# Performance work log

Hardware: AMD Instinct MI355X
Metric: run time of the kernel (lower is better)

Reference implementation:

```python
import jax, jax.numpy as jnp
import numpy as np

DIM = 256
NUM_HEADS = 4
HEAD_DIM = DIM // NUM_HEADS
EPS = 1e-5


def setup_inputs() -> dict:
    key = jax.random.key(0)
    ks = jax.random.split(key, 8)
    B, N, C = 8, 2048, DIM
    s = 0.02
    return {
        "x": jax.random.normal(ks[0], (B, N, C), jnp.float32),
        "qkv_w": jax.random.normal(ks[1], (C, 3 * C), jnp.float32) * s,
        "qkv_b": jnp.zeros((3 * C,), jnp.float32),
        "proj_w": jax.random.normal(ks[2], (C, C), jnp.float32) * s,
        "proj_b": jnp.zeros((C,), jnp.float32),
        "ln1_g": jnp.ones((C,), jnp.float32),
        "ln1_b": jnp.zeros((C,), jnp.float32),
        "ln2_g": jnp.ones((C,), jnp.float32),
        "ln2_b": jnp.zeros((C,), jnp.float32),
        "mlp_w1": jax.random.normal(ks[3], (C, 2 * C), jnp.float32) * s,
        "mlp_b1": jnp.zeros((2 * C,), jnp.float32),
        "mlp_w2": jax.random.normal(ks[4], (2 * C, C), jnp.float32) * s,
        "mlp_b2": jnp.zeros((C,), jnp.float32),
    }


def _layernorm(x, g, b):
    mu = jnp.mean(x, axis=-1, keepdims=True)
    var = jnp.mean(jnp.square(x - mu), axis=-1, keepdims=True)
    return (x - mu) * jax.lax.rsqrt(var + EPS) * g + b


def reference(x, qkv_w, qkv_b, proj_w, proj_b, ln1_g, ln1_b, ln2_g, ln2_b,
              mlp_w1, mlp_b1, mlp_w2, mlp_b2):
    B, N, C = x.shape
    H, D = NUM_HEADS, HEAD_DIM
    shortcut = x
    h = _layernorm(x, ln1_g, ln1_b)
    qkv = (h @ qkv_w + qkv_b).reshape(B, N, 3, H, D)
    q = qkv[:, :, 0].transpose(0, 2, 1, 3)  # [B,H,N,D]
    k = qkv[:, :, 1].transpose(0, 2, 1, 3)
    v = qkv[:, :, 2].transpose(0, 2, 1, 3)
    attn = jnp.einsum('bhnd,bhmd->bhnm', q, k) * (D ** -0.5)
    attn = jax.nn.softmax(attn, axis=-1)  # dropout = identity (eval mode)
    o = jnp.einsum('bhnm,bhmd->bhnd', attn, v)
    o = o.transpose(0, 2, 1, 3).reshape(B, N, C)
    x = o @ proj_w + proj_b + shortcut
    h2 = _layernorm(x, ln2_g, ln2_b)
    mlp = jax.nn.gelu(h2 @ mlp_w1 + mlp_b1, approximate=False) @ mlp_w2 + mlp_b2
    return x + mlp
```

## Files before the change

kernel.cpp:

```cpp
#include <hip/hip_runtime.h>

typedef __bf16 bf16;
typedef __bf16 bf16x8 __attribute__((ext_vector_type(8)));
typedef __bf16 bf16x4 __attribute__((ext_vector_type(4)));
typedef float  f32x4  __attribute__((ext_vector_type(4)));

typedef __attribute__((address_space(1))) const void GASV;
typedef __attribute__((address_space(3))) void LASV;

__device__ __forceinline__ void gload16(const void* g, void* l) {
  __builtin_amdgcn_global_load_lds((GASV*)g, (LASV*)l, 16, 0, 0);
}

__global__ __launch_bounds__(256) void wconv_t(const float* __restrict__ in,
                                               bf16* __restrict__ out,
                                               int lgK, int Cin, int total) {
  int idx = blockIdx.x * 256 + threadIdx.x;
  if (idx >= total) return;
  int K = 1 << lgK;
  int k = idx & (K - 1);
  int n = idx >> lgK;
  out[idx] = (bf16)in[(size_t)k * Cin + n];
}

__global__ __launch_bounds__(256) void ln_fwd(const float* __restrict__ x,
                                              const float* __restrict__ gam,
                                              const float* __restrict__ bet,
                                              bf16* __restrict__ out) {
  const int lane = threadIdx.x & 63;
  const int w = threadIdx.x >> 6;
  const size_t row = (size_t)blockIdx.x * 4 + w;
  const float4 v = *(const float4*)(x + row * 256 + lane * 4);
  float s1 = v.x + v.y + v.z + v.w;
  float s2 = v.x * v.x + v.y * v.y + v.z * v.z + v.w * v.w;
#pragma unroll
  for (int m = 1; m < 64; m <<= 1) {
    s1 += __shfl_xor(s1, m);
    s2 += __shfl_xor(s2, m);
  }
  const float mu = s1 * (1.0f / 256.0f);
  const float var = s2 * (1.0f / 256.0f) - mu * mu;
  const float rs = rsqrtf(var + 1e-5f);
  const float4 g4 = *(const float4*)(gam + lane * 4);
  const float4 b4 = *(const float4*)(bet + lane * 4);
  bf16x4 o;
  o[0] = (bf16)((v.x - mu) * rs * g4.x + b4.x);
  o[1] = (bf16)((v.y - mu) * rs * g4.y + b4.y);
  o[2] = (bf16)((v.z - mu) * rs * g4.z + b4.z);
  o[3] = (bf16)((v.w - mu) * rs * g4.w + b4.w);
  *(bf16x4*)(out + row * 256 + lane * 4) = o;
}

template <int EPI>
__global__ __launch_bounds__(256) void gemm_bt(const bf16* __restrict__ A,
                                               const bf16* __restrict__ Bt,
                                               const float* __restrict__ bias,
                                               const float* __restrict__ res,
                                               void* __restrict__ outp,
                                               int M, int N, int K) {
  __shared__ bf16 Al[2][8192];
  __shared__ bf16 Bl[2][8192];
  const int tid = threadIdx.x;
  const int lane = tid & 63;
  const int wid = tid >> 6;
  const int wm = wid >> 1, wn = wid & 1;
  const int nbm = M >> 7;
  const int bm = (int)blockIdx.x % nbm;
  const int bn = (int)blockIdx.x / nbm;
  const int m0 = bm << 7, n0 = bn << 7;
  const int nk = K >> 6;

  f32x4 acc[4][4];
#pragma unroll
  for (int i = 0; i < 4; ++i)
#pragma unroll
    for (int j = 0; j < 4; ++j) acc[i][j] = (f32x4){0.f, 0.f, 0.f, 0.f};

  auto stage = [&](int t, int s) {
    const int k0 = t << 6;
#pragma unroll
    for (int p = 0; p < 4; ++p) {
      const int idx = p * 4096 + tid * 16;
      const int row = idx >> 7;
      const int colb = idx & 127;
      gload16((const char*)(A + ((size_t)(m0 + row) * K + k0)) + colb,
              (char*)&Al[s][0] + p * 4096 + ((tid >> 6) << 10));
      gload16((const char*)(Bt + ((size_t)(n0 + row) * K + k0)) + colb,
              (char*)&Bl[s][0] + p * 4096 + ((tid >> 6) << 10));
    }
  };

  stage(0, 0);
  asm volatile("s_waitcnt vmcnt(0)" ::: "memory");
  __syncthreads();

  for (int t = 0; t < nk; ++t) {
    if (t + 1 < nk) stage(t + 1, (t + 1) & 1);
    const bf16* pa = &Al[t & 1][0] + (wm * 64 + (lane & 15)) * 64 + ((lane >> 4) << 3);
    const bf16* pb = &Bl[t & 1][0] + (wn * 64 + (lane & 15)) * 64 + ((lane >> 4) << 3);
    bf16x8 av[4][2], bv[4][2];
#pragma unroll
    for (int f = 0; f < 4; ++f)
#pragma unroll
      for (int ks = 0; ks < 2; ++ks) {
        av[f][ks] = *(const bf16x8*)(pa + f * 1024 + ks * 32);
        bv[f][ks] = *(const bf16x8*)(pb + f * 1024 + ks * 32);
      }
#pragma unroll
    for (int fm = 0; fm < 4; ++fm)
#pragma unroll
      for (int fn = 0; fn < 4; ++fn) {
        acc[fm][fn] = __builtin_amdgcn_mfma_f32_16x16x32_bf16(av[fm][0], bv[fn][0], acc[fm][fn], 0, 0, 0);
        acc[fm][fn] = __builtin_amdgcn_mfma_f32_16x16x32_bf16(av[fm][1], bv[fn][1], acc[fm][fn], 0, 0, 0);
      }
    asm volatile("s_waitcnt vmcnt(0)" ::: "memory");
    __syncthreads();
  }

#pragma unroll
  for (int fm = 0; fm < 4; ++fm)
#pragma unroll
    for (int fn = 0; fn < 4; ++fn) {
      const int r0 = m0 + wm * 64 + fm * 16 + ((lane >> 4) << 2);
      const int c = n0 + wn * 64 + fn * 16 + (lane & 15);
#pragma unroll
      for (int j = 0; j < 4; ++j) {
        const int r = r0 + j;
        const float v = acc[fm][fn][j];
        if constexpr (EPI == 0) {
          ((bf16*)outp)[(size_t)r * N + c] = (bf16)(v + bias[c]);
        } else if constexpr (EPI == 1) {
          ((bf16*)outp)[(size_t)r * 2048 + ((size_t)(c >> 11)) * 524288 + (c & 2047)] =
              (bf16)(v + bias[r]);
        } else if constexpr (EPI == 2) {
          ((float*)outp)[(size_t)r * N + c] = v + bias[c] + res[(size_t)r * N + c];
        } else {
          const float u = v + bias[c];
          ((bf16*)outp)[(size_t)r * N + c] = (bf16)(u * 0.5f * (1.0f + erff(u * 0.70710678118f)));
        }
      }
    }
}

__global__ __launch_bounds__(256) void attn_fwd(const bf16* __restrict__ qk,
                                                const bf16* __restrict__ vT,
                                                bf16* __restrict__ ob) {
  __shared__ bf16 Kl[2][4096];
  __shared__ bf16 Vl[2][4096];
  const int tid = threadIdx.x;
  const int lane = tid & 63;
  const int w = tid >> 6;
  const int g = lane >> 4;
  const int qi = lane & 15;
  const int bh = blockIdx.x & 31;
  const int qt = blockIdx.x >> 5;
  const int b = bh >> 2, h = bh & 3;

  const size_t qrow = (size_t)b * 2048 + qt * 64 + w * 16 + qi;
  const bf16* qp = qk + qrow * 512 + h * 64 + g * 8;
  const bf16x8 qf0 = *(const bf16x8*)qp;
  const bf16x8 qf1 = *(const bf16x8*)(qp + 32);

  float mrun = -1e30f, lsum = 0.0f;
  f32x4 o[4];
#pragma unroll
  for (int i = 0; i < 4; ++i) o[i] = (f32x4){0.f, 0.f, 0.f, 0.f};

  const char* kbase = (const char*)qk + ((size_t)b * 2048) * 1024 + 512 + h * 128;
  const char* vbase = (const char*)vT + (size_t)bh * 262144;
  constexpr float CEXP = 0.125f * 1.44269504088896340736f;

  auto stage = [&](int t, int s) {
#pragma unroll
    for (int p = 0; p < 4; ++p) {
      const int idx = (p & 1) * 4096 + tid * 16;
      const int row = idx >> 7;
      const int colb = (idx ^ ((row & 7) << 4)) & 127;
      if (p < 2) {
        gload16(kbase + (size_t)(t * 64 + row) * 1024 + colb,
                (char*)&Kl[s][0] + (p & 1) * 4096 + ((tid >> 6) << 10));
      } else {
        gload16(vbase + (size_t)row * 4096 + t * 128 + colb,
                (char*)&Vl[s][0] + (p & 1) * 4096 + ((tid >> 6) << 10));
      }
    }
  };

  stage(0, 0);
  asm volatile("s_waitcnt vmcnt(0)" ::: "memory");
  __syncthreads();

  for (int t = 0; t < 32; ++t) {
    if (t < 31) stage(t + 1, (t + 1) & 1);
    const int s = t & 1;
    f32x4 st[4];
#pragma unroll
    for (int fk = 0; fk < 4; ++fk) {
      const int kvr = fk * 16 + qi;
      const char* kb = (const char*)&Kl[s][0] + kvr * 128;
      const int sw = (kvr & 7) << 4;
      const bf16x8 k0 = *(const bf16x8*)(kb + ((g * 16) ^ sw));
      const bf16x8 k1 = *(const bf16x8*)(kb + ((64 + g * 16) ^ sw));
      f32x4 z = (f32x4){0.f, 0.f, 0.f, 0.f};
      st[fk] = __builtin_amdgcn_mfma_f32_16x16x32_bf16(k0, qf0, z, 0, 0, 0);
      st[fk] = __builtin_amdgcn_mfma_f32_16x16x32_bf16(k1, qf1, st[fk], 0, 0, 0);
    }
    float mt = st[0][0];
#pragma unroll
    for (int fk = 0; fk < 4; ++fk)
#pragma unroll
      for (int j = 0; j < 4; ++j) mt = fmaxf(mt, st[fk][j]);
    mt = fmaxf(mt, __shfl_xor(mt, 16));
    mt = fmaxf(mt, __shfl_xor(mt, 32));
    const float mnew = fmaxf(mrun, mt);
    const float alpha = exp2f(CEXP * (mrun - mnew));
    float p[16];
    float ts = 0.f;
#pragma unroll
    for (int fk = 0; fk < 4; ++fk)
#pragma unroll
      for (int j = 0; j < 4; ++j) {
        const float pv = exp2f(CEXP * (st[fk][j] - mnew));
        p[fk * 4 + j] = pv;
        ts += pv;
      }
    ts += __shfl_xor(ts, 16);
    ts += __shfl_xor(ts, 32);
    lsum = lsum * alpha + ts;
    mrun = mnew;
    float aj[4];
#pragma unroll
    for (int j = 0; j < 4; ++j) aj[j] = __shfl(alpha, g * 4 + j);
#pragma unroll
    for (int fd = 0; fd < 4; ++fd)
#pragma unroll
      for (int j = 0; j < 4; ++j) o[fd][j] *= aj[j];
    unsigned pk[8];
#pragma unroll
    for (int fk = 0; fk < 4; ++fk)
#pragma unroll
      for (int jp = 0; jp < 2; ++jp) {
        union { bf16 hh[2]; unsigned u; } cv;
        cv.hh[0] = (bf16)p[fk * 4 + 2 * jp];
        cv.hh[1] = (bf16)p[fk * 4 + 2 * jp + 1];
        pk[fk * 2 + jp] = cv.u;
      }
#pragma unroll
    for (int ksl = 0; ksl < 2; ++ksl) {
      union { bf16x8 v; unsigned u[4]; } pa;
#pragma unroll
      for (int pp = 0; pp < 4; ++pp) {
        const int src = ((2 * (g & 1) + (pp >> 1)) << 4) | qi;
        const unsigned r0 = (unsigned)__shfl((int)pk[(ksl * 2) * 2 + (pp & 1)], src);
        const unsigned r1 = (unsigned)__shfl((int)pk[(ksl * 2 + 1) * 2 + (pp & 1)], src);
        pa.u[pp] = (g >> 1) ? r1 : r0;
      }
#pragma unroll
      for (int fd = 0; fd < 4; ++fd) {
        const int dr = fd * 16 + qi;
        const char* vb = (const char*)&Vl[s][0] + dr * 128;
        const bf16x8 vv = *(const bf16x8*)(vb + ((ksl * 64 + g * 16) ^ ((dr & 7) << 4)));
        o[fd] = __builtin_amdgcn_mfma_f32_16x16x32_bf16(pa.v, vv, o[fd], 0, 0, 0);
      }
    }
    asm volatile("s_waitcnt vmcnt(0)" ::: "memory");
    __syncthreads();
  }

  const float inv = 1.0f / lsum;
  float ij[4];
#pragma unroll
  for (int j = 0; j < 4; ++j) ij[j] = __shfl(inv, g * 4 + j);
  const size_t orow0 = (size_t)b * 2048 + qt * 64 + w * 16 + g * 4;
#pragma unroll
  for (int fd = 0; fd < 4; ++fd)
#pragma unroll
    for (int j = 0; j < 4; ++j)
      ob[(orow0 + j) * 256 + h * 64 + fd * 16 + qi] = (bf16)(o[fd][j] * ij[j]);
}

extern "C" void kernel_launch(void* const* d_in, const int* in_sizes, int n_in,
                              void* d_out, int out_size, void* d_ws, size_t ws_size,
                              hipStream_t stream) {
  const float* x      = (const float*)d_in[0];
  const float* qkv_w  = (const float*)d_in[1];
  const float* qkv_b  = (const float*)d_in[2];
  const float* proj_w = (const float*)d_in[3];
  const float* proj_b = (const float*)d_in[4];
  const float* ln1_g  = (const float*)d_in[5];
  const float* ln1_b  = (const float*)d_in[6];
  const float* ln2_g  = (const float*)d_in[7];
  const float* ln2_b  = (const float*)d_in[8];
  const float* mlp_w1 = (const float*)d_in[9];
  const float* mlp_b1 = (const float*)d_in[10];
  const float* mlp_w2 = (const float*)d_in[11];
  const float* mlp_b2 = (const float*)d_in[12];
  float* out = (float*)d_out;

  char* ws = (char*)d_ws;
  bf16* Wtqkv = (bf16*)(ws);
  bf16* WtP   = (bf16*)(ws + 393216);
  bf16* Wt1   = (bf16*)(ws + 524288);
  bf16* Wt2   = (bf16*)(ws + 786432);
  bf16* h     = (bf16*)(ws + 1048576);
  bf16* qkb   = (bf16*)(ws + 9437184);
  bf16* vT    = (bf16*)(ws + 26214400);
  bf16* obuf  = (bf16*)(ws + 34603008);
  float* x2   = (float*)(ws + 42991616);
  bf16* a1 = qkb;
  bf16* h2 = h;

  wconv_t<<<768, 256, 0, stream>>>(qkv_w, Wtqkv, 8, 768, 196608);
  wconv_t<<<256, 256, 0, stream>>>(proj_w, WtP, 8, 256, 65536);
  wconv_t<<<512, 256, 0, stream>>>(mlp_w1, Wt1, 8, 512, 131072);
  wconv_t<<<512, 256, 0, stream>>>(mlp_w2, Wt2, 9, 256, 131072);

  ln_fwd<<<4096, 256, 0, stream>>>(x, ln1_g, ln1_b, h);
  gemm_bt<0><<<512, 256, 0, stream>>>(h, Wtqkv, qkv_b, nullptr, qkb, 16384, 512, 256);
  gemm_bt<1><<<256, 256, 0, stream>>>(Wtqkv + 512 * 256, h, qkv_b + 512, nullptr, vT, 256, 16384, 256);
  attn_fwd<<<1024, 256, 0, stream>>>(qkb, vT, obuf);
  gemm_bt<2><<<256, 256, 0, stream>>>(obuf, WtP, proj_b, x, x2, 16384, 256, 256);
  ln_fwd<<<4096, 256, 0, stream>>>(x2, ln2_g, ln2_b, h2);
  gemm_bt<3><<<512, 256, 0, stream>>>(h2, Wt1, mlp_b1, nullptr, a1, 16384, 512, 256);
  gemm_bt<2><<<256, 256, 0, stream>>>(a1, Wt2, mlp_b2, x2, out, 16384, 256, 512);
}
```

Before: 184.1 us.

## Restructure attention: transposed S layout, LDS P exchange, lazy rescale, MFMA priority

The attention kernel now computes S transposed so each lane owns one query column. That removes cross-lane shuffles for alpha and the final normalisation. P is passed through a per-wave LDS buffer instead of shuffle-based repacking, and K/V are staged into an MFMA-fragment-ordered LDS layout rather than an XOR-swizzled one. Online-softmax rescaling is skipped unless some row max grows past a threshold, and s_setprio is raised around MFMA blocks in both attention and GEMM. This adds LDS traffic and some numeric risk from deferred rescaling, which allows exponents up to 2^8 before bf16 conversion.

```diff
diff --git a/kernel.cpp b/kernel.cpp
--- a/kernel.cpp
+++ b/kernel.cpp
@@ -4,6 +4,7 @@
 typedef __bf16 bf16x8 __attribute__((ext_vector_type(8)));
 typedef __bf16 bf16x4 __attribute__((ext_vector_type(4)));
 typedef float  f32x4  __attribute__((ext_vector_type(4)));
+typedef unsigned u32x2 __attribute__((ext_vector_type(2)));
 
 typedef __attribute__((address_space(1))) const void GASV;
 typedef __attribute__((address_space(3))) void LASV;
@@ -106,6 +107,7 @@
         av[f][ks] = *(const bf16x8*)(pa + f * 1024 + ks * 32);
         bv[f][ks] = *(const bf16x8*)(pb + f * 1024 + ks * 32);
       }
+    __builtin_amdgcn_s_setprio(1);
 #pragma unroll
     for (int fm = 0; fm < 4; ++fm)
 #pragma unroll
@@ -113,6 +115,7 @@
         acc[fm][fn] = __builtin_amdgcn_mfma_f32_16x16x32_bf16(av[fm][0], bv[fn][0], acc[fm][fn], 0, 0, 0);
         acc[fm][fn] = __builtin_amdgcn_mfma_f32_16x16x32_bf16(av[fm][1], bv[fn][1], acc[fm][fn], 0, 0, 0);
       }
+    __builtin_amdgcn_s_setprio(0);
     asm volatile("s_waitcnt vmcnt(0)" ::: "memory");
     __syncthreads();
   }
@@ -147,6 +150,7 @@
                                                 bf16* __restrict__ ob) {
   __shared__ bf16 Kl[2][4096];
   __shared__ bf16 Vl[2][4096];
+  __shared__ bf16 Pl[4][1024];
   const int tid = threadIdx.x;
   const int lane = tid & 63;
   const int w = tid >> 6;
@@ -161,7 +165,7 @@
   const bf16x8 qf0 = *(const bf16x8*)qp;
   const bf16x8 qf1 = *(const bf16x8*)(qp + 32);
 
-  float mrun = -1e30f, lsum = 0.0f;
+  float mrun = 0.0f, lsum = 0.0f;
   f32x4 o[4];
 #pragma unroll
   for (int i = 0; i < 4; ++i) o[i] = (f32x4){0.f, 0.f, 0.f, 0.f};
@@ -169,20 +173,30 @@
   const char* kbase = (const char*)qk + ((size_t)b * 2048) * 1024 + 512 + h * 128;
   const char* vbase = (const char*)vT + (size_t)bh * 262144;
   constexpr float CEXP = 0.125f * 1.44269504088896340736f;
+  constexpr float THR = 8.0f / CEXP;
+
+  int koff[2], voff[2];
+#pragma unroll
+  for (int i = 0; i < 2; ++i) {
+    const int fk = i * 2 + (w >> 1);
+    const int half = w & 1;
+    koff[i] = (fk * 16 + qi) * 1024 + half * 64 + g * 16;
+    voff[i] = (fk * 16 + qi) * 4096 + half * 64 + g * 16;
+  }
+  char* const pw = (char*)&Pl[w][0];
+  int paddr[4];
+#pragma unroll
+  for (int fk = 0; fk < 4; ++fk)
+    paddr[fk] = (fk >> 1) * 1024 + ((fk & 1) * 2 + (g >> 1)) * 256 + qi * 16 + ((g & 1) * 2) * 4;
+  const char* const pr = (const char*)&Pl[w][0] + lane * 16;
 
   auto stage = [&](int t, int s) {
-#pragma unroll
-    for (int p = 0; p < 4; ++p) {
-      const int idx = (p & 1) * 4096 + tid * 16;
-      const int row = idx >> 7;
-      const int colb = (idx ^ ((row & 7) << 4)) & 127;
-      if (p < 2) {
-        gload16(kbase + (size_t)(t * 64 + row) * 1024 + colb,
-                (char*)&Kl[s][0] + (p & 1) * 4096 + ((tid >> 6) << 10));
-      } else {
-        gload16(vbase + (size_t)row * 4096 + t * 128 + colb,
-                (char*)&Vl[s][0] + (p & 1) * 4096 + ((tid >> 6) << 10));
-      }
+    const size_t kt = (size_t)t * 65536;
+    const size_t vt = (size_t)t * 128;
+#pragma unroll
+    for (int i = 0; i < 2; ++i) {
+      gload16(kbase + kt + koff[i], (char*)&Kl[s][0] + i * 4096 + w * 1024);
+      gload16(vbase + vt + voff[i], (char*)&Vl[s][0] + i * 4096 + w * 1024);
     }
   };
 
@@ -193,90 +207,85 @@
   for (int t = 0; t < 32; ++t) {
     if (t < 31) stage(t + 1, (t + 1) & 1);
     const int s = t & 1;
+    const char* kb = (const char*)&Kl[s][0] + lane * 16;
     f32x4 st[4];
+    __builtin_amdgcn_s_setprio(1);
 #pragma unroll
     for (int fk = 0; fk < 4; ++fk) {
-      const int kvr = fk * 16 + qi;
-      const char* kb = (const char*)&Kl[s][0] + kvr * 128;
-      const int sw = (kvr & 7) << 4;
-      const bf16x8 k0 = *(const bf16x8*)(kb + ((g * 16) ^ sw));
-      const bf16x8 k1 = *(const bf16x8*)(kb + ((64 + g * 16) ^ sw));
+      const bf16x8 k0 = *(const bf16x8*)(kb + fk * 2048);
+      const bf16x8 k1 = *(const bf16x8*)(kb + fk * 2048 + 1024);
       f32x4 z = (f32x4){0.f, 0.f, 0.f, 0.f};
       st[fk] = __builtin_amdgcn_mfma_f32_16x16x32_bf16(k0, qf0, z, 0, 0, 0);
       st[fk] = __builtin_amdgcn_mfma_f32_16x16x32_bf16(k1, qf1, st[fk], 0, 0, 0);
     }
-    float mt = st[0][0];
+    __builtin_amdgcn_s_setprio(0);
+    float pmax = st[0][0];
 #pragma unroll
     for (int fk = 0; fk < 4; ++fk)
 #pragma unroll
-      for (int j = 0; j < 4; ++j) mt = fmaxf(mt, st[fk][j]);
-    mt = fmaxf(mt, __shfl_xor(mt, 16));
-    mt = fmaxf(mt, __shfl_xor(mt, 32));
-    const float mnew = fmaxf(mrun, mt);
-    const float alpha = exp2f(CEXP * (mrun - mnew));
-    float p[16];
+      for (int j = 0; j < 4; ++j) pmax = fmaxf(pmax, st[fk][j]);
+    if (!__all(pmax <= mrun + THR)) {
+      float mt = fmaxf(pmax, __shfl_xor(pmax, 16));
+      mt = fmaxf(mt, __shfl_xor(mt, 32));
+      const float mnew = fmaxf(mrun, mt);
+      const float alpha = exp2f(CEXP * (mrun - mnew));
+      lsum *= alpha;
+#pragma unroll
+      for (int fd = 0; fd < 4; ++fd)
+#pragma unroll
+        for (int j = 0; j < 4; ++j) o[fd][j] *= alpha;
+      mrun = mnew;
+    }
+    const float negcm = -CEXP * mrun;
     float ts = 0.f;
+    unsigned pk[8];
 #pragma unroll
     for (int fk = 0; fk < 4; ++fk)
 #pragma unroll
-      for (int j = 0; j < 4; ++j) {
-        const float pv = exp2f(CEXP * (st[fk][j] - mnew));
-        p[fk * 4 + j] = pv;
-        ts += pv;
+      for (int jp = 0; jp < 2; ++jp) {
+        const float p0 = exp2f(fmaf(st[fk][2 * jp], CEXP, negcm));
+        const float p1 = exp2f(fmaf(st[fk][2 * jp + 1], CEXP, negcm));
+        ts += p0 + p1;
+        union { bf16 h2[2]; unsigned u; } cv;
+        cv.h2[0] = (bf16)p0;
+        cv.h2[1] = (bf16)p1;
+        pk[fk * 2 + jp] = cv.u;
       }
     ts += __shfl_xor(ts, 16);
     ts += __shfl_xor(ts, 32);
-    lsum = lsum * alpha + ts;
-    mrun = mnew;
-    float aj[4];
-#pragma unroll
-    for (int j = 0; j < 4; ++j) aj[j] = __shfl(alpha, g * 4 + j);
-#pragma unroll
-    for (int fd = 0; fd < 4; ++fd)
-#pragma unroll
-      for (int j = 0; j < 4; ++j) o[fd][j] *= aj[j];
-    unsigned pk[8];
-#pragma unroll
-    for (int fk = 0; fk < 4; ++fk)
-#pragma unroll
-      for (int jp = 0; jp < 2; ++jp) {
-        union { bf16 hh[2]; unsigned u; } cv;
-        cv.hh[0] = (bf16)p[fk * 4 + 2 * jp];
-        cv.hh[1] = (bf16)p[fk * 4 + 2 * jp + 1];
-        pk[fk * 2 + jp] = cv.u;
-      }
-#pragma unroll
-    for (int ksl = 0; ksl < 2; ++ksl) {
-      union { bf16x8 v; unsigned u[4]; } pa;
-#pragma unroll
-      for (int pp = 0; pp < 4; ++pp) {
-        const int src = ((2 * (g & 1) + (pp >> 1)) << 4) | qi;
-        const unsigned r0 = (unsigned)__shfl((int)pk[(ksl * 2) * 2 + (pp & 1)], src);
-        const unsigned r1 = (unsigned)__shfl((int)pk[(ksl * 2 + 1) * 2 + (pp & 1)], src);
-        pa.u[pp] = (g >> 1) ? r1 : r0;
-      }
-#pragma unroll
-      for (int fd = 0; fd < 4; ++fd) {
-        const int dr = fd * 16 + qi;
-        const char* vb = (const char*)&Vl[s][0] + dr * 128;
-        const bf16x8 vv = *(const bf16x8*)(vb + ((ksl * 64 + g * 16) ^ ((dr & 7) << 4)));
-        o[fd] = __builtin_amdgcn_mfma_f32_16x16x32_bf16(pa.v, vv, o[fd], 0, 0, 0);
-      }
-    }
+    lsum += ts;
+#pragma unroll
+    for (int fk = 0; fk < 4; ++fk) {
+      u32x2 pr2;
+      pr2[0] = pk[fk * 2];
+      pr2[1] = pk[fk * 2 + 1];
+      *(u32x2*)(pw + paddr[fk]) = pr2;
+    }
+    const bf16x8 pa0 = *(const bf16x8*)(pr);
+    const bf16x8 pa1 = *(const bf16x8*)(pr + 1024);
+    const char* vb = (const char*)&Vl[s][0] + lane * 16;
+    __builtin_amdgcn_s_setprio(1);
+#pragma unroll
+    for (int fd = 0; fd < 4; ++fd) {
+      const bf16x8 v0 = *(const bf16x8*)(vb + fd * 2048);
+      const bf16x8 v1 = *(const bf16x8*)(vb + fd * 2048 + 1024);
+      o[fd] = __builtin_amdgcn_mfma_f32_16x16x32_bf16(v0, pa0, o[fd], 0, 0, 0);
+      o[fd] = __builtin_amdgcn_mfma_f32_16x16x32_bf16(v1, pa1, o[fd], 0, 0, 0);
+    }
+    __builtin_amdgcn_s_setprio(0);
     asm volatile("s_waitcnt vmcnt(0)" ::: "memory");
     __syncthreads();
   }
 
   const float inv = 1.0f / lsum;
-  float ij[4];
-#pragma unroll
-  for (int j = 0; j < 4; ++j) ij[j] = __shfl(inv, g * 4 + j);
-  const size_t orow0 = (size_t)b * 2048 + qt * 64 + w * 16 + g * 4;
-#pragma unroll
-  for (int fd = 0; fd < 4; ++fd)
-#pragma unroll
-    for (int j = 0; j < 4; ++j)
-      ob[(orow0 + j) * 256 + h * 64 + fd * 16 + qi] = (bf16)(o[fd][j] * ij[j]);
+  bf16* const orow = ob + qrow * 256 + h * 64 + g * 4;
+#pragma unroll
+  for (int fd = 0; fd < 4; ++fd) {
+    bf16x4 ov;
+#pragma unroll
+    for (int j = 0; j < 4; ++j) ov[j] = (bf16)(o[fd][j] * inv);
+    *(bf16x4*)(orow + fd * 16) = ov;
+  }
 }
 
 extern "C" void kernel_launch(void* const* d_in, const int* in_sizes, int n_in,
```

After: 179.1 us. 1.03x faster.
